# Kernel optimization log

Hardware: AMD Instinct MI355X
Metric: run time of the kernel (lower is better)

## Reference

```python
import jax, jax.numpy as jnp
import numpy as np
import math

FACTOR = 5  # args.factor


def setup_inputs() -> dict:
    key = jax.random.key(0)
    kq, kk, kv, ki = jax.random.split(key, 4)
    B, L, H, D = 8, 2048, 8, 64
    sample_k = min(FACTOR * int(np.ceil(np.log(L))), L)  # 40
    return {
        "queries": jax.random.normal(kq, (B, L, H, D), dtype=jnp.float32),
        "keys": jax.random.normal(kk, (B, L, H, D), dtype=jnp.float32),
        "values": jax.random.normal(kv, (B, L, H, D), dtype=jnp.float32),
        "index_sample": jax.random.randint(ki, (L, sample_k), 0, L),
    }


def reference(queries, keys, values, index_sample):
    B, L_Q, H, D = queries.shape
    L_K = keys.shape[1]
    # [B, L, H, D] -> [B, H, L, D]
    Q = queries.transpose(0, 2, 1, 3)
    K = keys.transpose(0, 2, 1, 3)
    V = values.transpose(0, 2, 1, 3)

    u = min(FACTOR * int(np.ceil(np.log(L_Q))), L_Q)  # n_top

    # ---- _prob_QK: sampled scores + sparsity measure + top-u queries ----
    # gather sampled keys per query position: [B, H, L_Q, sample_k, D]
    K_sample = K[:, :, index_sample, :]
    Q_K_sample = jnp.einsum('bhqd,bhqsd->bhqs', Q, K_sample)  # [B,H,L_Q,S]
    M = Q_K_sample.max(-1) - Q_K_sample.mean(-1)              # [B,H,L_Q]
    _, M_top = jax.lax.top_k(M, u)                            # [B,H,u]

    Q_reduce = jnp.take_along_axis(Q, M_top[..., None], axis=2)  # [B,H,u,D]
    scores = jnp.einsum('bhud,bhkd->bhuk', Q_reduce, K) * (1.0 / math.sqrt(D))

    # ---- initial context: mean of V broadcast over queries ----
    context = jnp.broadcast_to(V.mean(axis=2, keepdims=True), (B, H, L_Q, D))

    # ---- update context at selected query positions ----
    attn = jax.nn.softmax(scores, axis=-1)                  # [B,H,u,L_K]
    ctx_upd = jnp.einsum('bhuk,bhkd->bhud', attn, V)        # [B,H,u,D]
    bi = jnp.arange(B)[:, None, None]
    hi = jnp.arange(H)[None, :, None]
    context = context.at[bi, hi, M_top].set(ctx_upd)

    # [B,H,L_Q,D] -> [B,L_Q,H*D]
    return context.transpose(0, 2, 1, 3).reshape(B, L_Q, H * D)
```

## Files before the change

### kernel.cpp

```cpp
#include <hip/hip_runtime.h>
#include <hip/hip_bf16.h>

#define BB 8
#define LL 2048
#define HH 8
#define DD 64
#define HD 512
#define SK 40
#define UU 40
#define NCHUNK 16
#define CHUNK 128

typedef float v4f __attribute__((ext_vector_type(4)));

static const size_t OFF_M     = 0;
static const size_t OFF_TOP   = 512ull * 1024;
static const size_t OFF_VPART = 592ull * 1024;
static const size_t OFF_MPART = 768ull * 1024;
static const size_t OFF_SPART = 960ull * 1024;
static const size_t OFF_OPART = 1152ull * 1024;

template <int CTRL>
__device__ __forceinline__ float dpp_add(float x) {
    int yi = __builtin_amdgcn_mov_dpp(__float_as_int(x), CTRL, 0xF, 0xF, true);
    return x + __int_as_float(yi);
}

#define KA_PF 10
__global__ __launch_bounds__(128, 4) void kA_sample_scores(
    const float* __restrict__ Q, const float* __restrict__ K,
    const int* __restrict__ IS, float* __restrict__ M)
{
    int blk = blockIdx.x;
    int b = blk & 7;
    int q = blk >> 3;
    int tid = threadIdx.x;
    int h = tid >> 4;
    int lane = tid & 15;

    const int* __restrict__ isq = IS + q * SK;
    size_t base = (size_t)b * LL * HD;
    int off = h * DD + lane * 4;
    v4f qv = __builtin_nontemporal_load(
        (const v4f*)(Q + base + (size_t)q * HD + off));
    const float* __restrict__ Kb = K + base;

    int sidx[SK];
#pragma unroll
    for (int s = 0; s < SK; ++s)
        sidx[s] = __builtin_amdgcn_readfirstlane(isq[s]);

    float4 kv[KA_PF];
#pragma unroll
    for (int i = 0; i < KA_PF; ++i)
        kv[i] = *(const float4*)(Kb + (size_t)sidx[i] * HD + off);

    float mx = -1e30f, sm = 0.f;
#pragma unroll
    for (int s = 0; s < SK; ++s) {
        float4 k = kv[s % KA_PF];
        if (s + KA_PF < SK)
            kv[s % KA_PF] = *(const float4*)(Kb + (size_t)sidx[s + KA_PF] * HD + off);
        float p = qv.x * k.x + qv.y * k.y + qv.z * k.z + qv.w * k.w;
        p = dpp_add<0xB1>(p);
        p = dpp_add<0x4E>(p);
        p = dpp_add<0x141>(p);
        p = dpp_add<0x140>(p);
        mx = fmaxf(mx, p);
        sm += p;
    }
    if (lane == 0)
        M[((size_t)(b * HH + h)) * LL + q] = mx - sm * (1.0f / SK);
}

__global__ __launch_bounds__(256) void kB_topk(
    const float* __restrict__ M, int* __restrict__ TopIdx)
{
    int bh = blockIdx.x;
    int tid = threadIdx.x;
    __shared__ unsigned keys[LL];
    __shared__ int      hist[4096];
    __shared__ int      sscan[256];
    __shared__ unsigned ckeyA[2048];
    __shared__ int      cidxA[2048];
    __shared__ unsigned ckeyB[2048];
    __shared__ int      cidxB[2048];
    __shared__ int ctr[8];

    const float* __restrict__ m = M + (size_t)bh * LL;
    for (int i = tid; i < 4096; i += 256) hist[i] = 0;
    if (tid < 8) ctr[tid] = 0;
    __syncthreads();

    for (int i = tid; i < LL; i += 256) {
        unsigned u = __float_as_uint(m[i]);
        u = (u & 0x80000000u) ? ~u : (u | 0x80000000u);
        keys[i] = u;
        atomicAdd(&hist[u >> 20], 1);
    }
    __syncthreads();
    {
        int p = 0;
#pragma unroll
        for (int j = 0; j < 16; ++j) p += hist[tid * 16 + j];
        sscan[tid] = p;
        __syncthreads();
        for (int o = 1; o < 256; o <<= 1) {
            int v = (tid + o < 256) ? sscan[tid + o] : 0;
            __syncthreads();
            sscan[tid] += v;
            __syncthreads();
        }
        int snext = (tid < 255) ? sscan[tid + 1] : 0;
        if (sscan[tid] >= UU && snext < UU) {
            int cum = snext;
            for (int bkt = tid * 16 + 15; bkt >= tid * 16; --bkt) {
                int c = hist[bkt];
                if (cum + c >= UU) { ctr[3] = bkt; ctr[4] = UU - cum; break; }
                cum += c;
            }
        }
    }
    __syncthreads();
    unsigned T1 = (unsigned)ctr[3];
    int k1 = ctr[4];
    for (int i = tid; i < LL; i += 256) {
        unsigned u = keys[i];
        unsigned bkt = u >> 20;
        if (bkt > T1) {
            int p = atomicAdd(&ctr[0], 1);
            TopIdx[bh * UU + p] = i;
        } else if (bkt == T1) {
            int p = atomicAdd(&ctr[1], 1);
            ckeyA[p] = u; cidxA[p] = i;
        }
    }
    __syncthreads();
    int nA = ctr[1];

    for (int i = tid; i < 4096; i += 256) hist[i] = 0;
    __syncthreads();
    for (int i = tid; i < nA; i += 256)
        atomicAdd(&hist[(ckeyA[i] >> 8) & 0xFFF], 1);
    __syncthreads();
    {
        int p = 0;
#pragma unroll
        for (int j = 0; j < 16; ++j) p += hist[tid * 16 + j];
        sscan[tid] = p;
        __syncthreads();
        for (int o = 1; o < 256; o <<= 1) {
            int v = (tid + o < 256) ? sscan[tid + o] : 0;
            __syncthreads();
            sscan[tid] += v;
            __syncthreads();
        }
        int snext = (tid < 255) ? sscan[tid + 1] : 0;
        if (sscan[tid] >= k1 && snext < k1) {
            int cum = snext;
            for (int bkt = tid * 16 + 15; bkt >= tid * 16; --bkt) {
                int c = hist[bkt];
                if (cum + c >= k1) { ctr[3] = bkt; ctr[4] = k1 - cum; break; }
                cum += c;
            }
        }
    }
    __syncthreads();
    unsigned T2 = (unsigned)ctr[3];
    int k2 = ctr[4];
    for (int i = tid; i < nA; i += 256) {
        unsigned u = ckeyA[i];
        unsigned bkt = (u >> 8) & 0xFFF;
        if (bkt > T2) {
            int p = atomicAdd(&ctr[0], 1);
            TopIdx[bh * UU + p] = cidxA[i];
        } else if (bkt == T2) {
            int p = atomicAdd(&ctr[2], 1);
            ckeyB[p] = u; cidxB[p] = cidxA[i];
        }
    }
    __syncthreads();
    int nB = ctr[2];

    for (int i = tid; i < 256; i += 256) hist[i] = 0;
    __syncthreads();
    for (int i = tid; i < nB; i += 256)
        atomicAdd(&hist[ckeyB[i] & 0xFF], 1);
    __syncthreads();
    {
        sscan[tid] = hist[tid];
        __syncthreads();
        for (int o = 1; o < 256; o <<= 1) {
            int v = (tid + o < 256) ? sscan[tid + o] : 0;
            __syncthreads();
            sscan[tid] += v;
            __syncthreads();
        }
        int snext = (tid < 255) ? sscan[tid + 1] : 0;
        if (sscan[tid] >= k2 && snext < k2) { ctr[3] = tid; ctr[4] = k2 - snext; }
    }
    __syncthreads();
    unsigned T3 = (unsigned)ctr[3];
    int k3 = ctr[4];
    for (int i = tid; i < nB; i += 256) {
        unsigned u = ckeyB[i];
        unsigned bkt = u & 0xFF;
        if (bkt > T3) {
            int p = atomicAdd(&ctr[0], 1);
            TopIdx[bh * UU + p] = cidxB[i];
        } else if (bkt == T3) {
            int p = atomicAdd(&ctr[5], 1);
            cidxA[p] = cidxB[i];
        }
    }
    __syncthreads();
    if (tid == 0) {
        int n = ctr[5];
        int basep = ctr[0];
        for (int r = 0; r < k3; ++r) {
            int bi = 1 << 30, bp = -1;
            for (int j = 0; j < n; ++j) {
                int id = cidxA[j];
                if (id >= 0 && id < bi) { bi = id; bp = j; }
            }
            TopIdx[bh * UU + basep + r] = bi;
            cidxA[bp] = -1;
        }
    }
}

__global__ __launch_bounds__(256) void kC_vmean(
    const float* __restrict__ V, float* __restrict__ Vpart)
{
    int bh = blockIdx.x >> 3;
    int ch = blockIdx.x & 7;
    int b = bh >> 3, h = bh & 7;
    int tid = threadIdx.x;
    int dq = tid & 15;
    int lg = tid >> 4;

    float4 acc = make_float4(0.f, 0.f, 0.f, 0.f);
    size_t base = ((size_t)b * LL + ch * 256) * HD + h * DD + dq * 4;
    for (int l = lg; l < 256; l += 16) {
        float4 v = *(const float4*)(V + base + (size_t)l * HD);
        acc.x += v.x; acc.y += v.y; acc.z += v.z; acc.w += v.w;
    }
    __shared__ float4 red[256];
    red[tid] = acc;
    __syncthreads();
    if (tid < 16) {
        float4 s = make_float4(0.f, 0.f, 0.f, 0.f);
#pragma unroll
        for (int g = 0; g < 16; ++g) {
            float4 v = red[g * 16 + tid];
            s.x += v.x; s.y += v.y; s.z += v.z; s.w += v.w;
        }
        *(float4*)(Vpart + ch * 4096 + bh * 64 + tid * 4) = s;
    }
}

__global__ __launch_bounds__(256) void kD_fill(
    const float* __restrict__ Vpart, float* __restrict__ out)
{
    size_t i4 = (size_t)blockIdx.x * 256 + threadIdx.x;
    size_t o = i4 * 4;
    int hd = (int)(o & (HD - 1));
    int b  = (int)(o >> 20);
    int h  = hd >> 6;
    int idx = (b * HH + h) * DD + (hd & 63);
    float4 acc = make_float4(0.f, 0.f, 0.f, 0.f);
#pragma unroll
    for (int c = 0; c < 8; ++c) {
        float4 v = *(const float4*)(Vpart + c * 4096 + idx);
        acc.x += v.x; acc.y += v.y; acc.z += v.z; acc.w += v.w;
    }
    const float sc = 1.0f / LL;
    float4 r; r.x = acc.x * sc; r.y = acc.y * sc; r.z = acc.z * sc; r.w = acc.w * sc;
    *(float4*)(out + o) = r;
}

__global__ __launch_bounds__(256, 4) void kE_attn_partial(
    const float* __restrict__ Q, const float* __restrict__ K, const float* __restrict__ V,
    const int* __restrict__ TopIdx,
    float* __restrict__ Opart, float* __restrict__ mpart, float* __restrict__ spart)
{
    int c  = blockIdx.x;
    int bh = blockIdx.y;
    int b = bh >> 3, h = bh & 7;
    int tid = threadIdx.x;

    __shared__ float Qs[UU * DD];
    __shared__ float PT[UU][CHUNK + 4];
    __shared__ int   qidx[UU];
    __shared__ float mred[UU], sred[UU];

    if (tid < UU) qidx[tid] = TopIdx[bh * UU + tid];
    __syncthreads();

    size_t hbase  = (size_t)b * LL * HD + h * DD;
    size_t kcbase = hbase + (size_t)c * CHUNK * HD;

    for (int r = tid; r < UU * 16; r += 256) {
        int u = r >> 4, j = r & 15;
        *(float4*)(Qs + u * DD + j * 4) =
            *(const float4*)(Q + hbase + (size_t)qidx[u] * HD + j * 4);
    }
    __syncthreads();

    {
        int w = tid >> 6;
        int lane = tid & 63;
        const float* __restrict__ K0 = K + kcbase + (size_t)lane * HD;
        const float* __restrict__ K1 = K0 + (size_t)64 * HD;

        float d0[10], d1[10];
#pragma unroll
        for (int i = 0; i < 10; ++i) { d0[i] = 0.f; d1[i] = 0.f; }

#pragma unroll 1
        for (int qt = 0; qt < 4; ++qt) {
            float4 ka[4], kb[4];
#pragma unroll
            for (int j = 0; j < 4; ++j) {
                ka[j] = *(const float4*)(K0 + qt * 16 + j * 4);
                kb[j] = *(const float4*)(K1 + qt * 16 + j * 4);
            }
#pragma unroll
            for (int j = 0; j < 4; ++j) {
#pragma unroll
                for (int uu = 0; uu < 10; ++uu) {
                    float4 qv = *(const float4*)(Qs + (w * 10 + uu) * DD + qt * 16 + j * 4);
                    d0[uu] += qv.x * ka[j].x + qv.y * ka[j].y + qv.z * ka[j].z + qv.w * ka[j].w;
                    d1[uu] += qv.x * kb[j].x + qv.y * kb[j].y + qv.z * kb[j].z + qv.w * kb[j].w;
                }
            }
        }

#pragma unroll
        for (int uu = 0; uu < 10; ++uu) {
            int u = w * 10 + uu;
            float x0 = d0[uu] * 0.125f;
            float x1 = d1[uu] * 0.125f;
            float m = fmaxf(x0, x1);
            m = fmaxf(m, __shfl_xor(m, 1));
            m = fmaxf(m, __shfl_xor(m, 2));
            m = fmaxf(m, __shfl_xor(m, 4));
            m = fmaxf(m, __shfl_xor(m, 8));
            m = fmaxf(m, __shfl_xor(m, 16));
            m = fmaxf(m, __shfl_xor(m, 32));
            float p0 = __expf(x0 - m);
            float p1 = __expf(x1 - m);
            PT[u][lane]      = p0;
            PT[u][lane + 64] = p1;
            float s = p0 + p1;
            s += __shfl_xor(s, 1);
            s += __shfl_xor(s, 2);
            s += __shfl_xor(s, 4);
            s += __shfl_xor(s, 8);
            s += __shfl_xor(s, 16);
            s += __shfl_xor(s, 32);
            if (lane == 0) { mred[u] = m; sred[u] = s; }
        }
    }
    __syncthreads();

    {
        int dq = tid & 15, ug4 = tid >> 4;
        float4 acc[3];
#pragma unroll
        for (int i = 0; i < 3; ++i) acc[i] = make_float4(0.f, 0.f, 0.f, 0.f);
        const float* __restrict__ Vb = V + kcbase + dq * 4;
        for (int l0 = 0; l0 < CHUNK; l0 += 8) {
            float4 v[8];
#pragma unroll
            for (int j = 0; j < 8; ++j)
                v[j] = *(const float4*)(Vb + (size_t)(l0 + j) * HD);
#pragma unroll
            for (int i = 0; i < 3; ++i) {
                int u = ug4 + 16 * i;
                if (u < UU) {
                    float4 pa = *(const float4*)(&PT[u][l0]);
                    float4 pb = *(const float4*)(&PT[u][l0 + 4]);
                    acc[i].x += pa.x * v[0].x + pa.y * v[1].x + pa.z * v[2].x + pa.w * v[3].x
                              + pb.x * v[4].x + pb.y * v[5].x + pb.z * v[6].x + pb.w * v[7].x;
                    acc[i].y += pa.x * v[0].y + pa.y * v[1].y + pa.z * v[2].y + pa.w * v[3].y
                              + pb.x * v[4].y + pb.y * v[5].y + pb.z * v[6].y + pb.w * v[7].y;
                    acc[i].z += pa.x * v[0].z + pa.y * v[1].z + pa.z * v[2].z + pa.w * v[3].z
                              + pb.x * v[4].z + pb.y * v[5].z + pb.z * v[6].z + pb.w * v[7].z;
                    acc[i].w += pa.x * v[0].w + pa.y * v[1].w + pa.z * v[2].w + pa.w * v[3].w
                              + pb.x * v[4].w + pb.y * v[5].w + pb.z * v[6].w + pb.w * v[7].w;
                }
            }
        }
#pragma unroll
        for (int i = 0; i < 3; ++i) {
            int u = ug4 + 16 * i;
            if (u < UU) {
                size_t ob = (((size_t)(bh * UU + u)) * NCHUNK + c) * DD + dq * 4;
                *(float4*)(Opart + ob) = acc[i];
            }
        }
    }
    if (tid < UU) {
        mpart[(bh * UU + tid) * NCHUNK + c] = mred[tid];
        spart[(bh * UU + tid) * NCHUNK + c] = sred[tid];
    }
}

__global__ __launch_bounds__(64) void kF_combine(
    const float* __restrict__ Opart, const float* __restrict__ mpart,
    const float* __restrict__ spart, const int* __restrict__ TopIdx,
    float* __restrict__ out)
{
    int g = blockIdx.x;
    int bh = g / UU;
    int b = bh >> 3, h = bh & 7;
    int d = threadIdx.x;

    float m_i[NCHUNK];
    float Mx = -1e30f;
#pragma unroll
    for (int i = 0; i < NCHUNK; ++i) { m_i[i] = mpart[g * NCHUNK + i]; Mx = fmaxf(Mx, m_i[i]); }
    float S = 0.f, O = 0.f;
#pragma unroll
    for (int i = 0; i < NCHUNK; ++i) {
        float w = __expf(m_i[i] - Mx);
        S += w * spart[g * NCHUNK + i];
        O += w * Opart[((size_t)g * NCHUNK + i) * DD + d];
    }
    int qi = TopIdx[g];
    out[((size_t)b * LL + qi) * HD + h * DD + d] = O / S;
}

extern "C" void kernel_launch(void* const* d_in, const int* in_sizes, int n_in,
                              void* d_out, int out_size, void* d_ws, size_t ws_size,
                              hipStream_t stream) {
    const float* Q  = (const float*)d_in[0];
    const float* K  = (const float*)d_in[1];
    const float* V  = (const float*)d_in[2];
    const int*   IS = (const int*)d_in[3];
    float* out = (float*)d_out;
    char* ws = (char*)d_ws;

    float* M      = (float*)(ws + OFF_M);
    int*   TopIdx = (int*)(ws + OFF_TOP);
    float* Vpart  = (float*)(ws + OFF_VPART);
    float* mpart  = (float*)(ws + OFF_MPART);
    float* spart  = (float*)(ws + OFF_SPART);
    float* Opart  = (float*)(ws + OFF_OPART);

    kA_sample_scores<<<BB * LL, 128, 0, stream>>>(Q, K, IS, M);
    kC_vmean<<<BB * HH * 8, 256, 0, stream>>>(V, Vpart);
    kB_topk<<<BB * HH, 256, 0, stream>>>(M, TopIdx);
    kD_fill<<<(BB * LL * HD) / (256 * 4), 256, 0, stream>>>(Vpart, out);
    kE_attn_partial<<<dim3(NCHUNK, BB * HH), 256, 0, stream>>>(Q, K, V, TopIdx,
                                                               Opart, mpart, spart);
    kF_combine<<<BB * HH * UU, 64, 0, stream>>>(Opart, mpart, spart, TopIdx, out);
}
```

Before: 245.2 us.

## Split sampled-score kernel across four waves with 8-lane per-head dot products

The sample-score kernel now runs 256 threads per block. Each of the four waves handles 10 of the 40 sampled keys, and 8 lanes per head each load two float4s per key. The per-wave max and sum are combined through shared memory with a barrier. The aim is more memory-level parallelism and shorter per-thread serial chains for the gathered K rows, at the cost of a __syncthreads, a shared-memory reduction, and less prefetch depth per wave.

```diff
diff --git a/kernel.cpp b/kernel.cpp
--- a/kernel.cpp
+++ b/kernel.cpp
@@ -26,8 +26,7 @@
     return x + __int_as_float(yi);
 }
 
-#define KA_PF 10
-__global__ __launch_bounds__(128, 4) void kA_sample_scores(
+__global__ __launch_bounds__(256, 4) void kA_sample_scores(
     const float* __restrict__ Q, const float* __restrict__ K,
     const int* __restrict__ IS, float* __restrict__ M)
 {
@@ -35,42 +34,51 @@
     int b = blk & 7;
     int q = blk >> 3;
     int tid = threadIdx.x;
-    int h = tid >> 4;
-    int lane = tid & 15;
+    int wv = tid >> 6;
+    int h  = (tid >> 3) & 7;
+    int ln = tid & 7;
 
     const int* __restrict__ isq = IS + q * SK;
     size_t base = (size_t)b * LL * HD;
-    int off = h * DD + lane * 4;
-    v4f qv = __builtin_nontemporal_load(
-        (const v4f*)(Q + base + (size_t)q * HD + off));
+    int off = h * DD + ln * 8;
+    const float* __restrict__ Qr = Q + base + (size_t)q * HD + off;
+    float4 qa = *(const float4*)Qr;
+    float4 qb = *(const float4*)(Qr + 4);
     const float* __restrict__ Kb = K + base;
 
-    int sidx[SK];
-#pragma unroll
-    for (int s = 0; s < SK; ++s)
-        sidx[s] = __builtin_amdgcn_readfirstlane(isq[s]);
-
-    float4 kv[KA_PF];
-#pragma unroll
-    for (int i = 0; i < KA_PF; ++i)
-        kv[i] = *(const float4*)(Kb + (size_t)sidx[i] * HD + off);
-
     float mx = -1e30f, sm = 0.f;
-#pragma unroll
-    for (int s = 0; s < SK; ++s) {
-        float4 k = kv[s % KA_PF];
-        if (s + KA_PF < SK)
-            kv[s % KA_PF] = *(const float4*)(Kb + (size_t)sidx[s + KA_PF] * HD + off);
-        float p = qv.x * k.x + qv.y * k.y + qv.z * k.z + qv.w * k.w;
-        p = dpp_add<0xB1>(p);
-        p = dpp_add<0x4E>(p);
-        p = dpp_add<0x141>(p);
-        p = dpp_add<0x140>(p);
-        mx = fmaxf(mx, p);
-        sm += p;
-    }
-    if (lane == 0)
-        M[((size_t)(b * HH + h)) * LL + q] = mx - sm * (1.0f / SK);
+    int sb = wv * 10;
+#pragma unroll
+    for (int bt = 0; bt < 2; ++bt) {
+        float4 ka[5], kb5[5];
+#pragma unroll
+        for (int i = 0; i < 5; ++i) {
+            int idx = __builtin_amdgcn_readfirstlane(isq[sb + bt * 5 + i]);
+            const float* __restrict__ r = Kb + (size_t)idx * HD + off;
+            ka[i]  = *(const float4*)r;
+            kb5[i] = *(const float4*)(r + 4);
+        }
+#pragma unroll
+        for (int i = 0; i < 5; ++i) {
+            float p = qa.x * ka[i].x + qa.y * ka[i].y + qa.z * ka[i].z + qa.w * ka[i].w
+                    + qb.x * kb5[i].x + qb.y * kb5[i].y + qb.z * kb5[i].z + qb.w * kb5[i].w;
+            p = dpp_add<0xB1>(p);
+            p = dpp_add<0x4E>(p);
+            p = dpp_add<0x141>(p);
+            mx = fmaxf(mx, p);
+            sm += p;
+        }
+    }
+
+    __shared__ float wmx[4][8], wsm[4][8];
+    if (ln == 0) { wmx[wv][h] = mx; wsm[wv][h] = sm; }
+    __syncthreads();
+    if (tid < 8) {
+        float m0 = fmaxf(fmaxf(wmx[0][tid], wmx[1][tid]),
+                         fmaxf(wmx[2][tid], wmx[3][tid]));
+        float s0 = wsm[0][tid] + wsm[1][tid] + wsm[2][tid] + wsm[3][tid];
+        M[((size_t)(b * HH + tid)) * LL + q] = m0 - s0 * (1.0f / SK);
+    }
 }
 
 __global__ __launch_bounds__(256) void kB_topk(
@@ -449,7 +457,7 @@
     float* spart  = (float*)(ws + OFF_SPART);
     float* Opart  = (float*)(ws + OFF_OPART);
 
-    kA_sample_scores<<<BB * LL, 128, 0, stream>>>(Q, K, IS, M);
+    kA_sample_scores<<<BB * LL, 256, 0, stream>>>(Q, K, IS, M);
     kC_vmean<<<BB * HH * 8, 256, 0, stream>>>(V, Vpart);
     kB_topk<<<BB * HH, 256, 0, stream>>>(M, TopIdx);
     kD_fill<<<(BB * LL * HD) / (256 * 4), 256, 0, stream>>>(Vpart, out);
```

Measured after the change: 255.9 us. 1.04x slower.
